# Kernel optimization log

Hardware: AMD Instinct MI355X
Metric: run time of the kernel (lower is better)

The kernel has to match this reference:

```python
import jax, jax.numpy as jnp
import numpy as np

T, B, H, I = 128, 128, 256, 256


def setup_inputs() -> dict:
    key = jax.random.key(0)
    ks = jax.random.split(key, 8)
    s = 1.0 / np.sqrt(H)
    embs = jax.random.normal(ks[0], (T, B, I), jnp.float32)
    # lens in [1, T] (a length of 0 is meaningless for this module)
    lens = jnp.maximum(jax.random.randint(ks[1], (B,), 0, T + 1), 1)
    Wih = jax.random.uniform(ks[2], (4 * H, I), jnp.float32, -s, s)
    Whh = jax.random.uniform(ks[3], (4 * H, H), jnp.float32, -s, s)
    bih = jax.random.uniform(ks[4], (4 * H,), jnp.float32, -s, s)
    bhh = jax.random.uniform(ks[5], (4 * H,), jnp.float32, -s, s)
    Wa = jax.random.uniform(ks[6], (H, 2 * H), jnp.float32, -s, s)
    ba = jnp.zeros((H,), jnp.float32)
    return {"embs": embs, "lens": lens, "Wih": Wih, "Whh": Whh,
            "bih": bih, "bhh": bhh, "Wa": Wa, "ba": ba}


def _forward(embs, Wih, Whh, bih, bhh, Wa, ba):
    Tn, Bn, _ = embs.shape
    Hn = Whh.shape[1]
    h0 = jnp.zeros((Bn, Hn), embs.dtype)
    c0 = jnp.zeros((Bn, Hn), embs.dtype)
    hids0 = jnp.zeros((Tn, Bn, Hn), embs.dtype)  # growing history of outputs
    pos = jnp.arange(Tn)

    def step(carry, emb):
        h, c, hids, t = carry
        # attention of current hidden over all previous outputs (dot-product scores)
        scores = jnp.einsum('bh,tbh->tb', h, hids)          # [T,B]
        valid = pos[:, None] < jnp.maximum(t, 1)             # at least one valid slot avoids NaN
        scores = jnp.where(valid, scores, -1e30)
        w = jax.nn.softmax(scores, axis=0)
        ctx = jnp.einsum('tb,tbh->bh', w, hids)              # [B,H]
        h_att = jnp.tanh(jnp.concatenate([h, ctx], axis=-1) @ Wa.T + ba)
        h_in = jnp.where(t > 0, h_att, h)                    # no attention before first output
        # one LSTM cell step (PyTorch gate order: i, f, g, o)
        gates = emb @ Wih.T + bih + h_in @ Whh.T + bhh       # [B,4H]
        i, f, g, o = jnp.split(gates, 4, axis=-1)
        c_new = jax.nn.sigmoid(f) * c + jax.nn.sigmoid(i) * jnp.tanh(g)
        h_new = jax.nn.sigmoid(o) * jnp.tanh(c_new)
        hids = jax.lax.dynamic_update_slice(hids, h_new[None], (t, 0, 0))
        return (h_new, c_new, hids, t + 1), (h_new, c_new)

    _, (hs, cs) = jax.lax.scan(step, (h0, c0, hids0, jnp.int32(0)), embs)
    return hs, cs  # each [T,B,H]


def reference(embs, lens, Wih, Whh, bih, bhh, Wa, ba):
    hs, cs = _forward(embs, Wih, Whh, bih, bhh, Wa, ba)
    bidx = jnp.arange(hs.shape[1])
    h_fin = hs[lens - 1, bidx][None]  # [1,B,H], state at t == len-1
    c_fin = cs[lens - 1, bidx][None]
    return hs, h_fin, c_fin
```

## Files before the change

### kernel.cpp

```cpp
#include <hip/hip_runtime.h>
#include <math.h>

#define T 128
#define B 128
#define H 256
#define I 256
#define G4 1024
#define NB 2

typedef unsigned short u16;
typedef unsigned int u32;
typedef _Float16 half_t;
typedef _Float16 half2_t __attribute__((ext_vector_type(2)));

#if defined(__has_builtin)
#if __has_builtin(__builtin_amdgcn_fdot2)
#define HAS_FDOT2 1
#endif
#endif

__device__ __forceinline__ float fdot2(half2_t a, half2_t b, float c) {
#ifdef HAS_FDOT2
    return __builtin_amdgcn_fdot2(a, b, c, false);
#else
    return fmaf((float)a.x, (float)b.x, fmaf((float)a.y, (float)b.y, c));
#endif
}
__device__ __forceinline__ half2_t h2cast(u32 u) { return __builtin_bit_cast(half2_t, u); }

__device__ __forceinline__ float sigmoid_fast(float x) {
    return 1.0f / (1.0f + __expf(-x));
}
__device__ __forceinline__ float tanh_fast(float x) {
    x = fminf(fmaxf(x, -15.f), 15.f);
    const float e = __expf(2.0f * x);
    return (e - 1.0f) / (e + 1.0f);
}

__global__ void pack_whH(const float* __restrict__ Whh, half2_t* __restrict__ WhH) {
    const int k2 = blockIdx.x;
    const int o  = threadIdx.x;
    half2_t v;
    v.x = (half_t)Whh[(size_t)o * H + 2 * k2];
    v.y = (half_t)Whh[(size_t)o * H + 2 * k2 + 1];
    WhH[(size_t)k2 * G4 + o] = v;
}
__global__ void pack_waH(const float* __restrict__ Wa, half2_t* __restrict__ WaH) {
    const int k2 = blockIdx.x;
    const int j  = threadIdx.x;
    half2_t v;
    v.x = (half_t)Wa[(size_t)j * (2 * H) + 2 * k2];
    v.y = (half_t)Wa[(size_t)j * (2 * H) + 2 * k2 + 1];
    WaH[(size_t)k2 * H + j] = v;
}

__global__ __launch_bounds__(256) void gemm_g(const float* __restrict__ A,
                                              const float* __restrict__ W,
                                              const float* __restrict__ bih,
                                              const float* __restrict__ bhh,
                                              float* __restrict__ G) {
    __shared__ __align__(16) float As[64][68];
    __shared__ __align__(16) float Ws[64][68];
    const int m0 = blockIdx.x * 64;
    const int n0 = blockIdx.y * 64;
    const int tid = threadIdx.x;
    const int ty = tid >> 4, tx = tid & 15;
    const int rr = tid >> 4;
    const int kr = tid & 15;

    float acc[4][4] = {};
    for (int k0 = 0; k0 < I; k0 += 64) {
#pragma unroll
        for (int i = 0; i < 4; ++i) {
            const int r = rr + 16 * i;
            const float4 av = *(const float4*)&A[(size_t)(m0 + r) * I + k0 + kr * 4];
            const float4 wv = *(const float4*)&W[(size_t)(n0 + r) * I + k0 + kr * 4];
            As[kr * 4 + 0][r] = av.x; As[kr * 4 + 1][r] = av.y;
            As[kr * 4 + 2][r] = av.z; As[kr * 4 + 3][r] = av.w;
            Ws[kr * 4 + 0][r] = wv.x; Ws[kr * 4 + 1][r] = wv.y;
            Ws[kr * 4 + 2][r] = wv.z; Ws[kr * 4 + 3][r] = wv.w;
        }
        __syncthreads();
#pragma unroll 8
        for (int kk = 0; kk < 64; ++kk) {
            const float4 a4 = *(const float4*)&As[kk][ty * 4];
            const float4 w4 = *(const float4*)&Ws[kk][tx * 4];
            const float a[4] = {a4.x, a4.y, a4.z, a4.w};
            const float w[4] = {w4.x, w4.y, w4.z, w4.w};
#pragma unroll
            for (int i = 0; i < 4; ++i)
#pragma unroll
                for (int jj = 0; jj < 4; ++jj)
                    acc[i][jj] = fmaf(a[i], w[jj], acc[i][jj]);
        }
        __syncthreads();
    }
    const int n = n0 + tx * 4;
    const float4 bi = *(const float4*)&bih[n];
    const float4 bh = *(const float4*)&bhh[n];
    const float4 bb = make_float4(bi.x + bh.x, bi.y + bh.y, bi.z + bh.z, bi.w + bh.w);
#pragma unroll
    for (int i = 0; i < 4; ++i) {
        const int m = m0 + ty * 4 + i;
        float4 o = make_float4(acc[i][0] + bb.x, acc[i][1] + bb.y,
                               acc[i][2] + bb.z, acc[i][3] + bb.w);
        *(float4*)&G[(size_t)m * G4 + n] = o;
    }
}

__global__ __launch_bounds__(1024, 4) void alstm4(
    const int* __restrict__ lens,
    const float* __restrict__ G,
    const half2_t* __restrict__ WhH,
    const half2_t* __restrict__ WaH,
    const float* __restrict__ ba,
    float* __restrict__ out)
{
    __shared__ __align__(16) half_t hid_s[NB][T][H];
    __shared__ __align__(16) float  sc_s[NB][T];
    __shared__ __align__(16) half_t hH_s[NB][H];
    __shared__ __align__(16) half_t hcI_s[4 * 256];
    __shared__ __align__(16) half_t hinI_s[4 * 128];
    __shared__ __align__(16) float  red_s[2048];
    __shared__ __align__(16) float  gate_s[NB][G4];

    const int b0 = blockIdx.x * NB;
    const int tid = threadIdx.x;
    const int lane = tid & 63;
    const int wave = tid >> 6;
    const int sb = wave >> 3;
    const int stp0 = wave & 7;
    const int cb = tid >> 9;
    const int ck = (tid >> 8) & 1;
    const int cj = tid & 255;
    const int ako = tid >> 8;
    const int aj = tid & 255;
    const int eb = tid >> 8;
    const int ej = tid & 255;

    const int len0 = lens[b0], len1 = lens[b0 + 1];
    float c_reg = 0.f;
    float* hfin = out + (size_t)T * B * H;
    float* cfin = hfin + (size_t)B * H;
    if (tid < 512) hH_s[eb][ej] = (half_t)0.f;
    __syncthreads();

    for (int t = 0; t < T; ++t) {
        const float gA = G[((size_t)t * B + b0) * G4 + tid];
        const float gB = G[((size_t)t * B + b0 + 1) * G4 + tid];

        if (t > 0) {
            const half2_t h2a = h2cast(*(const u32*)&hH_s[sb][lane * 4]);
            const half2_t h2b = h2cast(*(const u32*)&hH_s[sb][lane * 4 + 2]);
            for (int tp = stp0; tp < t; tp += 8) {
                const uint2 hv = *(const uint2*)&hid_s[sb][tp][lane * 4];
                float d = fdot2(h2cast(hv.x), h2a, fdot2(h2cast(hv.y), h2b, 0.f));
#pragma unroll
                for (int off = 32; off; off >>= 1) d += __shfl_xor(d, off);
                if (lane == 0) sc_s[sb][tp] = d;
            }
            __syncthreads();
            if (stp0 == 0) {
                const float v0 = (lane < t) ? sc_s[sb][lane] : -3.0e38f;
                const float v1 = (lane + 64 < t) ? sc_s[sb][lane + 64] : -3.0e38f;
                float m = fmaxf(v0, v1);
#pragma unroll
                for (int off = 32; off; off >>= 1) m = fmaxf(m, __shfl_xor(m, off));
                const float e0 = (lane < t) ? __expf(v0 - m) : 0.f;
                const float e1 = (lane + 64 < t) ? __expf(v1 - m) : 0.f;
                float s = e0 + e1;
#pragma unroll
                for (int off = 32; off; off >>= 1) s += __shfl_xor(s, off);
                const float inv = 1.f / s;
                if (lane < t) sc_s[sb][lane] = e0 * inv;
                if (lane + 64 < t) sc_s[sb][lane + 64] = e1 * inv;
            }
            __syncthreads();
            {
                float cacc = 0.f;
                for (int tp = ck; tp < t; tp += 2)
                    cacc = fmaf(sc_s[cb][tp], (float)hid_s[cb][tp][cj], cacc);
                red_s[cb * 512 + ck * 256 + cj] = cacc;
                gate_s[0][tid] = gA;
                gate_s[1][tid] = gB;
            }
            __syncthreads();
            if (tid < 512) {
                const float ctxv = red_s[eb * 512 + ej] + red_s[eb * 512 + 256 + ej];
                hcI_s[512 + 4 * (ej >> 1) + 2 * eb + (ej & 1)] = (half_t)ctxv;
            }
            __syncthreads();
            {
                const half2_t* wp = &WaH[(size_t)(ako * 64) * H + aj];
                float a0 = 0.f, a1 = 0.f;
#pragma unroll 8
                for (int kk = 0; kk < 64; ++kk) {
                    const int k2 = ako * 64 + kk;
                    const uint2 hh = *(const uint2*)&hcI_s[4 * k2];
                    const half2_t w = wp[(size_t)kk * H];
                    a0 = fdot2(w, h2cast(hh.x), a0);
                    a1 = fdot2(w, h2cast(hh.y), a1);
                }
                red_s[ako * 512 + aj] = a0;
                red_s[ako * 512 + 256 + aj] = a1;
            }
            __syncthreads();
            if (tid < 512) {
                float a = ba[ej];
#pragma unroll
                for (int r = 0; r < 4; ++r) a += red_s[r * 512 + eb * 256 + ej];
                hinI_s[4 * (ej >> 1) + 2 * eb + (ej & 1)] = (half_t)tanh_fast(a);
            }
            __syncthreads();
        } else {
            gate_s[0][tid] = gA;
            gate_s[1][tid] = gB;
            if (tid < 512) hinI_s[tid] = (half_t)0.f;
            __syncthreads();
        }
        {
            const half2_t* wp = &WhH[tid];
            float g0 = 0.f, g1 = 0.f;
#pragma unroll 8
            for (int k2 = 0; k2 < 128; ++k2) {
                const uint2 hh = *(const uint2*)&hinI_s[4 * k2];
                const half2_t w = wp[(size_t)k2 * G4];
                g0 = fdot2(w, h2cast(hh.x), g0);
                g1 = fdot2(w, h2cast(hh.y), g1);
            }
            red_s[tid] = g0;
            red_s[1024 + tid] = g1;
        }
        __syncthreads();
        if (tid < 512) {
            const int bg = b0 + eb;
            const float gi = gate_s[eb][ej]           + red_s[eb * 1024 + ej];
            const float gf = gate_s[eb][H + ej]       + red_s[eb * 1024 + H + ej];
            const float gg = gate_s[eb][2 * H + ej]   + red_s[eb * 1024 + 2 * H + ej];
            const float go = gate_s[eb][3 * H + ej]   + red_s[eb * 1024 + 3 * H + ej];
            const float ig = sigmoid_fast(gi);
            const float fg = sigmoid_fast(gf);
            const float gv = tanh_fast(gg);
            const float og = sigmoid_fast(go);
            c_reg = fmaf(fg, c_reg, ig * gv);
            const float h_new = og * tanh_fast(c_reg);
            const half_t hh = (half_t)h_new;
            hH_s[eb][ej] = hh;
            hid_s[eb][t][ej] = hh;
            hcI_s[4 * (ej >> 1) + 2 * eb + (ej & 1)] = hh;
            out[((size_t)t * B + bg) * H + ej] = h_new;
            const int lb = eb ? len1 : len0;
            if (t == lb - 1) {
                hfin[(size_t)bg * H + ej] = h_new;
                cfin[(size_t)bg * H + ej] = c_reg;
            }
        }
        __syncthreads();
    }
}

extern "C" void kernel_launch(void* const* d_in, const int* in_sizes, int n_in,
                              void* d_out, int out_size, void* d_ws, size_t ws_size,
                              hipStream_t stream) {
    const float* embs = (const float*)d_in[0];
    const int*   lens = (const int*)d_in[1];
    const float* Wih  = (const float*)d_in[2];
    const float* Whh  = (const float*)d_in[3];
    const float* bih  = (const float*)d_in[4];
    const float* bhh  = (const float*)d_in[5];
    const float* Wa   = (const float*)d_in[6];
    const float* ba   = (const float*)d_in[7];
    float* out = (float*)d_out;

    float* G      = (float*)d_ws;
    half2_t* WhH  = (half2_t*)(G + (size_t)T * B * G4);
    half2_t* WaH  = WhH + (size_t)128 * G4;

    pack_whH<<<128, G4, 0, stream>>>(Whh, WhH);
    pack_waH<<<256, H, 0, stream>>>(Wa, WaH);
    dim3 ggrid(T * B / 64, G4 / 64);
    gemm_g<<<ggrid, 256, 0, stream>>>(embs, Wih, bih, bhh, G);
    alstm4<<<B / NB, 1024, 0, stream>>>(lens, G, WhH, WaH, ba, out);
}
```

Baseline: 1.886 ms.

## Repack recurrent weights row-major and prefetch them into registers ahead of barriers

Weights for the recurrent and attention projections are repacked so each thread owns a contiguous row, letting it fetch 16-byte vectors. The first eight chunks are prefetched into a register ring before the preceding barrier or softmax phase, and the rest stream in during the dot loop. Gate preactivations are loaded straight into registers per cell instead of staged through shared memory. __syncthreads is replaced with a custom barrier that waits only on LDS counters, so the global prefetches can stay in flight across it. The cost is higher register pressure and reliance on hand-ordered waitcnt semantics.

```diff
diff --git a/kernel.cpp b/kernel.cpp
--- a/kernel.cpp
+++ b/kernel.cpp
@@ -37,21 +37,28 @@
     return (e - 1.0f) / (e + 1.0f);
 }
 
-__global__ void pack_whH(const float* __restrict__ Whh, half2_t* __restrict__ WhH) {
-    const int k2 = blockIdx.x;
-    const int o  = threadIdx.x;
+#define BAR() do {                                                  \
+    asm volatile("s_waitcnt lgkmcnt(0)" ::: "memory");              \
+    __builtin_amdgcn_s_barrier();                                   \
+    asm volatile("" ::: "memory");                                  \
+    __builtin_amdgcn_sched_barrier(0);                              \
+} while (0)
+
+__global__ void pack_whO(const float* __restrict__ Whh, half2_t* __restrict__ WhO) {
+    const int o  = blockIdx.x;
+    const int k2 = threadIdx.x;
     half2_t v;
     v.x = (half_t)Whh[(size_t)o * H + 2 * k2];
     v.y = (half_t)Whh[(size_t)o * H + 2 * k2 + 1];
-    WhH[(size_t)k2 * G4 + o] = v;
-}
-__global__ void pack_waH(const float* __restrict__ Wa, half2_t* __restrict__ WaH) {
-    const int k2 = blockIdx.x;
-    const int j  = threadIdx.x;
+    WhO[(size_t)o * 128 + k2] = v;
+}
+__global__ void pack_waO(const float* __restrict__ Wa, half2_t* __restrict__ WaO) {
+    const int j  = blockIdx.x;
+    const int k2 = threadIdx.x;
     half2_t v;
     v.x = (half_t)Wa[(size_t)j * (2 * H) + 2 * k2];
     v.y = (half_t)Wa[(size_t)j * (2 * H) + 2 * k2 + 1];
-    WaH[(size_t)k2 * H + j] = v;
+    WaO[(size_t)j * 256 + k2] = v;
 }
 
 __global__ __launch_bounds__(256) void gemm_g(const float* __restrict__ A,
@@ -108,21 +115,20 @@
     }
 }
 
-__global__ __launch_bounds__(1024, 4) void alstm4(
+__global__ __launch_bounds__(1024, 4) void alstm5(
     const int* __restrict__ lens,
     const float* __restrict__ G,
-    const half2_t* __restrict__ WhH,
-    const half2_t* __restrict__ WaH,
+    const half2_t* __restrict__ WhO,
+    const half2_t* __restrict__ WaO,
     const float* __restrict__ ba,
     float* __restrict__ out)
 {
     __shared__ __align__(16) half_t hid_s[NB][T][H];
     __shared__ __align__(16) float  sc_s[NB][T];
     __shared__ __align__(16) half_t hH_s[NB][H];
-    __shared__ __align__(16) half_t hcI_s[4 * 256];
-    __shared__ __align__(16) half_t hinI_s[4 * 128];
+    __shared__ __align__(16) half_t hcI_s[1024];
+    __shared__ __align__(16) half_t hinI_s[512];
     __shared__ __align__(16) float  red_s[2048];
-    __shared__ __align__(16) float  gate_s[NB][G4];
 
     const int b0 = blockIdx.x * NB;
     const int tid = threadIdx.x;
@@ -143,23 +149,37 @@
     float* hfin = out + (size_t)T * B * H;
     float* cfin = hfin + (size_t)B * H;
     if (tid < 512) hH_s[eb][ej] = (half_t)0.f;
-    __syncthreads();
+
+    const uint4* wrow  = (const uint4*)(WhO + (size_t)tid * 128);
+    const uint4* warow = (const uint4*)(WaO + (size_t)aj * 256 + (size_t)ako * 64);
+    const uint4* hinv  = (const uint4*)hinI_s;
+    const uint4* hcIv  = (const uint4*)hcI_s;
+
+    BAR();
 
     for (int t = 0; t < T; ++t) {
-        const float gA = G[((size_t)t * B + b0) * G4 + tid];
-        const float gB = G[((size_t)t * B + b0 + 1) * G4 + tid];
+        float gpi = 0.f, gpf = 0.f, gpg = 0.f, gpo = 0.f;
+        if (tid < 512) {
+            const float* gb = G + ((size_t)t * B + b0 + eb) * G4 + ej;
+            gpi = gb[0]; gpf = gb[H]; gpg = gb[2 * H]; gpo = gb[3 * H];
+        }
 
         if (t > 0) {
-            const half2_t h2a = h2cast(*(const u32*)&hH_s[sb][lane * 4]);
-            const half2_t h2b = h2cast(*(const u32*)&hH_s[sb][lane * 4 + 2]);
-            for (int tp = stp0; tp < t; tp += 8) {
-                const uint2 hv = *(const uint2*)&hid_s[sb][tp][lane * 4];
-                float d = fdot2(h2cast(hv.x), h2a, fdot2(h2cast(hv.y), h2b, 0.f));
-#pragma unroll
-                for (int off = 32; off; off >>= 1) d += __shfl_xor(d, off);
-                if (lane == 0) sc_s[sb][tp] = d;
-            }
-            __syncthreads();
+            uint4 wa_buf[8];
+#pragma unroll
+            for (int p = 0; p < 8; ++p) wa_buf[p] = warow[p];
+            {
+                const half2_t h2a = h2cast(*(const u32*)&hH_s[sb][lane * 4]);
+                const half2_t h2b = h2cast(*(const u32*)&hH_s[sb][lane * 4 + 2]);
+                for (int tp = stp0; tp < t; tp += 8) {
+                    const uint2 hv = *(const uint2*)&hid_s[sb][tp][lane * 4];
+                    float d = fdot2(h2cast(hv.x), h2a, fdot2(h2cast(hv.y), h2b, 0.f));
+#pragma unroll
+                    for (int off = 32; off; off >>= 1) d += __shfl_xor(d, off);
+                    if (lane == 0) sc_s[sb][tp] = d;
+                }
+            }
+            BAR();
             if (stp0 == 0) {
                 const float v0 = (lane < t) ? sc_s[sb][lane] : -3.0e38f;
                 const float v1 = (lane + 64 < t) ? sc_s[sb][lane + 64] : -3.0e38f;
@@ -175,73 +195,85 @@
                 if (lane < t) sc_s[sb][lane] = e0 * inv;
                 if (lane + 64 < t) sc_s[sb][lane + 64] = e1 * inv;
             }
-            __syncthreads();
+            BAR();
             {
                 float cacc = 0.f;
                 for (int tp = ck; tp < t; tp += 2)
                     cacc = fmaf(sc_s[cb][tp], (float)hid_s[cb][tp][cj], cacc);
                 red_s[cb * 512 + ck * 256 + cj] = cacc;
-                gate_s[0][tid] = gA;
-                gate_s[1][tid] = gB;
-            }
-            __syncthreads();
+            }
+            BAR();
             if (tid < 512) {
                 const float ctxv = red_s[eb * 512 + ej] + red_s[eb * 512 + 256 + ej];
                 hcI_s[512 + 4 * (ej >> 1) + 2 * eb + (ej & 1)] = (half_t)ctxv;
             }
-            __syncthreads();
+            BAR();
             {
-                const half2_t* wp = &WaH[(size_t)(ako * 64) * H + aj];
                 float a0 = 0.f, a1 = 0.f;
-#pragma unroll 8
-                for (int kk = 0; kk < 64; ++kk) {
-                    const int k2 = ako * 64 + kk;
-                    const uint2 hh = *(const uint2*)&hcI_s[4 * k2];
-                    const half2_t w = wp[(size_t)kk * H];
-                    a0 = fdot2(w, h2cast(hh.x), a0);
-                    a1 = fdot2(w, h2cast(hh.y), a1);
+#pragma unroll
+                for (int gg = 0; gg < 16; ++gg) {
+                    const uint4 w = wa_buf[gg & 7];
+                    if (gg + 8 < 16) wa_buf[gg & 7] = warow[gg + 8];
+                    const uint4 ha = hcIv[ako * 32 + 2 * gg];
+                    const uint4 hb = hcIv[ako * 32 + 2 * gg + 1];
+                    a0 = fdot2(h2cast(w.x), h2cast(ha.x), a0);
+                    a1 = fdot2(h2cast(w.x), h2cast(ha.y), a1);
+                    a0 = fdot2(h2cast(w.y), h2cast(ha.z), a0);
+                    a1 = fdot2(h2cast(w.y), h2cast(ha.w), a1);
+                    a0 = fdot2(h2cast(w.z), h2cast(hb.x), a0);
+                    a1 = fdot2(h2cast(w.z), h2cast(hb.y), a1);
+                    a0 = fdot2(h2cast(w.w), h2cast(hb.z), a0);
+                    a1 = fdot2(h2cast(w.w), h2cast(hb.w), a1);
                 }
                 red_s[ako * 512 + aj] = a0;
                 red_s[ako * 512 + 256 + aj] = a1;
             }
-            __syncthreads();
+            BAR();
+            uint4 wh_buf[8];
+#pragma unroll
+            for (int p = 0; p < 8; ++p) wh_buf[p] = wrow[p];
             if (tid < 512) {
                 float a = ba[ej];
 #pragma unroll
                 for (int r = 0; r < 4; ++r) a += red_s[r * 512 + eb * 256 + ej];
                 hinI_s[4 * (ej >> 1) + 2 * eb + (ej & 1)] = (half_t)tanh_fast(a);
             }
-            __syncthreads();
+            BAR();
+            {
+                float g0 = 0.f, g1 = 0.f;
+#pragma unroll
+                for (int gi = 0; gi < 32; ++gi) {
+                    const uint4 w = wh_buf[gi & 7];
+                    if (gi + 8 < 32) wh_buf[gi & 7] = wrow[gi + 8];
+                    const uint4 ha = hinv[2 * gi];
+                    const uint4 hb = hinv[2 * gi + 1];
+                    g0 = fdot2(h2cast(w.x), h2cast(ha.x), g0);
+                    g1 = fdot2(h2cast(w.x), h2cast(ha.y), g1);
+                    g0 = fdot2(h2cast(w.y), h2cast(ha.z), g0);
+                    g1 = fdot2(h2cast(w.y), h2cast(ha.w), g1);
+                    g0 = fdot2(h2cast(w.z), h2cast(hb.x), g0);
+                    g1 = fdot2(h2cast(w.z), h2cast(hb.y), g1);
+                    g0 = fdot2(h2cast(w.w), h2cast(hb.z), g0);
+                    g1 = fdot2(h2cast(w.w), h2cast(hb.w), g1);
+                }
+                red_s[tid] = g0;
+                red_s[1024 + tid] = g1;
+            }
         } else {
-            gate_s[0][tid] = gA;
-            gate_s[1][tid] = gB;
-            if (tid < 512) hinI_s[tid] = (half_t)0.f;
-            __syncthreads();
-        }
-        {
-            const half2_t* wp = &WhH[tid];
-            float g0 = 0.f, g1 = 0.f;
-#pragma unroll 8
-            for (int k2 = 0; k2 < 128; ++k2) {
-                const uint2 hh = *(const uint2*)&hinI_s[4 * k2];
-                const half2_t w = wp[(size_t)k2 * G4];
-                g0 = fdot2(w, h2cast(hh.x), g0);
-                g1 = fdot2(w, h2cast(hh.y), g1);
-            }
-            red_s[tid] = g0;
-            red_s[1024 + tid] = g1;
-        }
-        __syncthreads();
+            red_s[tid] = 0.f;
+            red_s[1024 + tid] = 0.f;
+        }
+        BAR();
         if (tid < 512) {
             const int bg = b0 + eb;
-            const float gi = gate_s[eb][ej]           + red_s[eb * 1024 + ej];
-            const float gf = gate_s[eb][H + ej]       + red_s[eb * 1024 + H + ej];
-            const float gg = gate_s[eb][2 * H + ej]   + red_s[eb * 1024 + 2 * H + ej];
-            const float go = gate_s[eb][3 * H + ej]   + red_s[eb * 1024 + 3 * H + ej];
-            const float ig = sigmoid_fast(gi);
-            const float fg = sigmoid_fast(gf);
-            const float gv = tanh_fast(gg);
-            const float og = sigmoid_fast(go);
+            const float gi_v = gpi + red_s[eb * 1024 + ej];
+            const float gf_v = gpf + red_s[eb * 1024 + H + ej];
+            const float gg_v = gpg + red_s[eb * 1024 + 2 * H + ej];
+            const float go_v = gpo + red_s[eb * 1024 + 3 * H + ej];
+            const float ig = sigmoid_fast(gi_v);
+            const float fg = sigmoid_fast(gf_v);
+            const float gv = tanh_fast(gg_v);
+            const float og = sigmoid_fast(go_v);
             c_reg = fmaf(fg, c_reg, ig * gv);
             const float h_new = og * tanh_fast(c_reg);
             const half_t hh = (half_t)h_new;
@@ -255,7 +287,7 @@
                 cfin[(size_t)bg * H + ej] = c_reg;
             }
         }
-        __syncthreads();
+        BAR();
     }
 }
 
@@ -273,12 +305,12 @@
     float* out = (float*)d_out;
 
     float* G      = (float*)d_ws;
-    half2_t* WhH  = (half2_t*)(G + (size_t)T * B * G4);
-    half2_t* WaH  = WhH + (size_t)128 * G4;
-
-    pack_whH<<<128, G4, 0, stream>>>(Whh, WhH);
-    pack_waH<<<256, H, 0, stream>>>(Wa, WaH);
+    half2_t* WhO  = (half2_t*)(G + (size_t)T * B * G4);
+    half2_t* WaO  = WhO + (size_t)1024 * 128;
+
+    pack_whO<<<G4, 128, 0, stream>>>(Whh, WhO);
+    pack_waO<<<H, 256, 0, stream>>>(Wa, WaO);
     dim3 ggrid(T * B / 64, G4 / 64);
     gemm_g<<<ggrid, 256, 0, stream>>>(embs, Wih, bih, bhh, G);
-    alstm4<<<B / NB, 1024, 0, stream>>>(lens, G, WhH, WaH, ba, out);
-}
+    alstm5<<<B / NB, 1024, 0, stream>>>(lens, G, WhO, WaO, ba, out);
+}
```

After: 3.636 ms. 92.8% more time.
